# Kernel tuning notes

Hardware: AMD Instinct MI355X
Metric: run time of the kernel (lower is better)

## Reference

```python
import jax, jax.numpy as jnp
import numpy as np

N = 50000; E = 1600000; H = 128; R = 8; T = 2; P = 1000; M = 223


def setup_inputs() -> dict:
    key = jax.random.key(0)
    ks = jax.random.split(key, 16)
    s = 1.0 / np.sqrt(H).astype(np.float32)
    inp = {}
    inp['neigh_type_count'] = jax.random.uniform(ks[0], (N, 2), dtype=jnp.float32) * 5.0
    inp['norm'] = jax.random.uniform(ks[1], (E,), dtype=jnp.float32) + 0.1
    inp['special_cost'] = jax.random.uniform(ks[2], (N,), dtype=jnp.float32)
    inp['gt_map'] = jax.random.uniform(ks[3], (M, M), dtype=jnp.float32)
    inp['fc_w'] = jax.random.normal(ks[4], (2, H), dtype=jnp.float32) * (1.0 / np.sqrt(2.0))
    inp['fc_b'] = jnp.zeros((H,), jnp.float32)
    inp['w_nt'] = jax.random.normal(ks[5], (T, H, H), dtype=jnp.float32) * s
    inp['w_rel'] = jax.random.normal(ks[6], (R, H, H), dtype=jnp.float32) * s
    inp['fc2_w'] = jax.random.normal(ks[7], (H, 1), dtype=jnp.float32) * s
    inp['fc2_b'] = jnp.zeros((1,), jnp.float32)
    inp['fc3_w'] = jax.random.normal(ks[8], (H, 1), dtype=jnp.float32) * s
    inp['fc3_b'] = jnp.zeros((1,), jnp.float32)
    inp['fl3_w'] = jax.random.normal(ks[9], (H, P), dtype=jnp.float32) * s
    inp['fl3_b'] = jnp.zeros((P,), jnp.float32)
    inp['node_type'] = jax.random.randint(ks[10], (N,), 0, T, dtype=jnp.int32)
    inp['src'] = jax.random.randint(ks[11], (E,), 0, N, dtype=jnp.int32)
    inp['dst'] = jax.random.randint(ks[12], (E,), 0, N, dtype=jnp.int32)
    inp['etype'] = jax.random.randint(ks[13], (E,), 0, R, dtype=jnp.int32)
    return inp


def reference(neigh_type_count, norm, special_cost, gt_map, fc_w, fc_b, w_nt, w_rel,
              fc2_w, fc2_b, fc3_w, fc3_b, fl3_w, fl3_b, node_type, src, dst, etype):
    n = neigh_type_count.shape[0]
    # fc: [N,2] -> [N,H]
    h0 = neigh_type_count @ fc_w + fc_b
    # input RGCN layer: per-src-node-type transform, then per-edge-relation transform.
    # Compute node x type / node x relation products once, then gather per edge
    # (same math as per-edge bmm with gathered weights, far less traffic).
    h_nt_all = jnp.einsum('ni,tio->nto', h0, w_nt)                 # [N,T,H]
    h_nt = jnp.take_along_axis(h_nt_all, node_type[:, None, None].astype(jnp.int32), axis=1)[:, 0, :]  # [N,H]
    h_rel = jnp.einsum('ni,rio->nro', h_nt, w_rel)                 # [N,R,H]
    msg = h_rel[src, etype] * norm[:, None]                        # [E,H]
    h = jax.ops.segment_sum(msg, dst, num_segments=n)              # scatter-sum -> [N,H]
    h = jax.nn.relu(h)                                             # apply_func activation
    # fc2 + clamp(sigmoid)
    pred = jnp.clip(jax.nn.sigmoid(h @ fc2_w + fc2_b), 1e-7, 1e10) # [N,1]
    m = gt_map.shape[0]
    pm = pred[:m * m, 0].reshape(m, m)                             # pred node map [M,M]
    ce = -jnp.sum(gt_map * jnp.log2(pm))                           # min cross-entropy (single GT map)
    rs = jnp.sum(pm, axis=1)                                       # row sums [M]
    cs = jnp.sum(pm, axis=0)                                       # col sums [M]
    loss2 = jnp.sum(pm * (rs[:, None] - pm)) + jnp.sum(pm * (cs[None, :] - pm))
    sumone = jnp.sum((rs - 1.0) ** 2) + jnp.sum((cs - 1.0) ** 2)
    # fc_for_loss3 (sigmoid probs; summed so params get grads)
    prob3_sum = jnp.sum(jax.nn.sigmoid(h @ fl3_w + fl3_b))
    # OutputLayer: scatter-sum src pred_prob to dst, (sum-1)^2 * special_cost
    agg = jax.ops.segment_sum(pred[src, 0], dst, num_segments=n)
    out_cost = jnp.sum(((agg - 1.0) ** 2) * special_cost)
    # dgl.mean_nodes (single graph) + fc3
    gembed = jnp.mean(h, axis=0)
    pred_obj = (gembed @ fc3_w + fc3_b)[0]
    return jnp.stack([pred_obj, sumone, loss2, ce, out_cost, prob3_sum])
```

## Files before the change

### kernel.cpp

```cpp
#include <hip/hip_runtime.h>

#define H 128
#define RNUM 8
#define TNUM 2
#define PNUM 1000
#define MNUM 223
#define BNODES 64
#define NBUCK 782
#define BCAP 2304
#define EPB 8192

typedef __attribute__((ext_vector_type(8))) short bf16x8;
typedef __attribute__((ext_vector_type(4))) float f32x4;

__device__ __forceinline__ float fsig(float z) {
    return 1.0f / (1.0f + __expf(-z));
}
__device__ __forceinline__ float fsig_fast(float z) {
    return __builtin_amdgcn_rcpf(1.0f + __expf(-z));
}

__device__ __forceinline__ float wave_reduce(float v) {
#pragma unroll
    for (int off = 32; off > 0; off >>= 1) v += __shfl_down(v, off, 64);
    return v;
}

__device__ __forceinline__ unsigned short f2bf(float f) {
    unsigned int u = __float_as_uint(f);
    u += 0x7fffu + ((u >> 16) & 1u);
    return (unsigned short)(u >> 16);
}

__global__ void setup_kernel(const float* __restrict__ fl3_w, const float* __restrict__ fl3_b,
                             unsigned short* __restrict__ wt, float* __restrict__ biasws,
                             const float* __restrict__ fc_w, const float* __restrict__ fc_b,
                             const float* __restrict__ w_nt, const float* __restrict__ w_rel,
                             float* __restrict__ C) {
    __shared__ float G[3][H];
    int blk = blockIdx.x;
    int i = threadIdx.x;
    if (blk < 1024) {
        int p = blk;
        float v = (p < PNUM) ? fl3_w[(size_t)i * PNUM + p] : 0.0f;
        wt[(size_t)p * H + i] = f2bf(v);
        if (i == 0) biasws[p] = (p < PNUM) ? fl3_b[p] : -1.0e4f;
        return;
    }
    int tr = blk - 1024;
    int t = tr >> 3, r = tr & 7;
    float a0 = 0.f, a1 = 0.f, a2 = 0.f;
#pragma unroll 8
    for (int j = 0; j < H; ++j) {
        float w = w_nt[((size_t)t * H + j) * H + i];
        a0 += fc_w[j] * w;
        a1 += fc_w[H + j] * w;
        a2 += fc_b[j] * w;
    }
    G[0][i] = a0; G[1][i] = a1; G[2][i] = a2;
    __syncthreads();
    float c0 = 0.f, c1 = 0.f, c2 = 0.f;
#pragma unroll 8
    for (int k = 0; k < H; ++k) {
        float w = w_rel[((size_t)r * H + k) * H + i];
        c0 += G[0][k] * w;
        c1 += G[1][k] * w;
        c2 += G[2][k] * w;
    }
    C[((size_t)tr * 3 + 0) * H + i] = c0;
    C[((size_t)tr * 3 + 1) * H + i] = c1;
    C[((size_t)tr * 3 + 2) * H + i] = c2;
}

__global__ void cbt_kernel(const float* __restrict__ C, unsigned short* __restrict__ CbT) {
    int o = blockIdx.x;
    int k = threadIdx.x;
    CbT[o * 64 + k] = (k < 48) ? f2bf(C[k * 128 + o]) : (unsigned short)0;
}

__global__ __launch_bounds__(1024) void partition_kernel(
        const int* __restrict__ src, const int* __restrict__ dst,
        const int* __restrict__ etype, const float* __restrict__ norm,
        const int* __restrict__ node_type, int* __restrict__ cursor,
        uint2* __restrict__ buck, int E) {
    __shared__ int lh[NBUCK];
    __shared__ int gb[NBUCK];
    int tid = threadIdx.x;
    for (int i = tid; i < NBUCK; i += 1024) lh[i] = 0;
    __syncthreads();
    int base = blockIdx.x * EPB;
    uint2 pl[8]; int bb[8]; int rk[8];
#pragma unroll
    for (int c = 0; c < 8; ++c) {
        int e = base + c * 1024 + tid;
        bb[c] = -1;
        if (e < E) {
            int s = src[e];
            int d = dst[e];
            int r = etype[e];
            float nm = norm[e];
            int t = node_type[s];
            int b = d >> 6;
            int local = d & 63;
            pl[c].x = (unsigned)s | ((unsigned)local << 18) | ((unsigned)r << 24) | ((unsigned)t << 27);
            pl[c].y = __float_as_uint(nm);
            bb[c] = b;
            rk[c] = atomicAdd(&lh[b], 1);
        }
    }
    __syncthreads();
    for (int i = tid; i < NBUCK; i += 1024) {
        if (lh[i] > 0) {
            int g = atomicAdd(&cursor[i], lh[i]);
            gb[i] = (g < 0) ? 0 : (g > BCAP ? BCAP : g);
        }
    }
    __syncthreads();
#pragma unroll
    for (int c = 0; c < 8; ++c) {
        if (bb[c] >= 0) {
            int pos = gb[bb[c]] + rk[c];
            if (pos < BCAP) buck[(size_t)bb[c] * BCAP + pos] = pl[c];
        }
    }
}

__global__ __launch_bounds__(256) void bucket_node(
        const uint2* __restrict__ buck, const int* __restrict__ cursor,
        const float* __restrict__ ntc, const unsigned short* __restrict__ CbT,
        const float* __restrict__ fc2_w, const float* __restrict__ fc2_b,
        unsigned short* __restrict__ hb, float* __restrict__ pred,
        float* __restrict__ gpart, int N) {
    __shared__ float S[64 * 68];
    __shared__ unsigned short Cb[128 * 72];
    __shared__ float gloc[128];
    int tid = threadIdx.x;
    int bkt = blockIdx.x;
    for (int i = tid; i < 64 * 68; i += 256) S[i] = 0.0f;
    for (int g = tid; g < 1024; g += 256) {
        int row = g >> 3, c = g & 7;
        uint4 v = ((const uint4*)CbT)[g];
        *(uint4*)(Cb + row * 72 + c * 8) = v;
    }
    if (tid < 128) gloc[tid] = 0.0f;
    __syncthreads();

    int cnt = cursor[bkt];
    if (cnt > BCAP) cnt = BCAP;
    if (cnt < 0) cnt = 0;
    const uint2* bp = buck + (size_t)bkt * BCAP;
    for (int base = 0; base < cnt; base += 2048) {
        uint2 pl[8]; float2 cc[8]; int ii[8];
#pragma unroll
        for (int j = 0; j < 8; ++j) {
            ii[j] = base + j * 256 + tid;
            pl[j] = (ii[j] < cnt) ? bp[ii[j]] : make_uint2(0u, 0u);
        }
#pragma unroll
        for (int j = 0; j < 8; ++j)
            cc[j] = (ii[j] < cnt) ? ((const float2*)ntc)[pl[j].x & 0x3FFFF]
                                  : make_float2(0.f, 0.f);
#pragma unroll
        for (int j = 0; j < 8; ++j) {
            if (ii[j] < cnt) {
                int local = (pl[j].x >> 18) & 63;
                int tr = ((pl[j].x >> 24) & 7) + (((pl[j].x >> 27) & 1) << 3);
                float nm = __uint_as_float(pl[j].y);
                float* p = &S[local * 68 + tr * 3];
                atomicAdd(p, nm * cc[j].x);
                atomicAdd(p + 1, nm * cc[j].y);
                atomicAdd(p + 2, nm);
            }
        }
    }
    __syncthreads();

    int lane = tid & 63, w = tid >> 6;
    int lrow = lane & 15, quad = lane >> 4;

    bf16x8 a[2];
#pragma unroll
    for (int ks = 0; ks < 2; ++ks) {
        const float* sp = S + (w * 16 + lrow) * 68 + ks * 32 + quad * 8;
        float4 f0 = *(const float4*)sp;
        float4 f1 = *(const float4*)(sp + 4);
        bf16x8 t;
        t[0] = (short)f2bf(f0.x); t[1] = (short)f2bf(f0.y);
        t[2] = (short)f2bf(f0.z); t[3] = (short)f2bf(f0.w);
        t[4] = (short)f2bf(f1.x); t[5] = (short)f2bf(f1.y);
        t[6] = (short)f2bf(f1.z); t[7] = (short)f2bf(f1.w);
        a[ks] = t;
    }

    f32x4 acc[8];
#pragma unroll
    for (int tn = 0; tn < 8; ++tn) acc[tn] = (f32x4){0.f, 0.f, 0.f, 0.f};
#pragma unroll
    for (int ks = 0; ks < 2; ++ks) {
#pragma unroll
        for (int tn = 0; tn < 8; ++tn) {
            bf16x8 b = *(const bf16x8*)(Cb + (tn * 16 + lrow) * 72 + ks * 32 + quad * 8);
            acc[tn] = __builtin_amdgcn_mfma_f32_16x16x32_bf16(a[ks], b, acc[tn], 0, 0, 0);
        }
    }

#pragma unroll
    for (int tn = 0; tn < 8; ++tn)
#pragma unroll
        for (int r = 0; r < 4; ++r) acc[tn][r] = fmaxf(acc[tn][r], 0.f);

    int vbase = bkt * BNODES + w * 16 + quad * 4;
#pragma unroll
    for (int r = 0; r < 4; ++r) {
        unsigned short* hrow = hb + (size_t)(vbase + r) * H + lrow;
#pragma unroll
        for (int tn = 0; tn < 8; ++tn) hrow[tn * 16] = f2bf(acc[tn][r]);
    }
    float pd[4];
#pragma unroll
    for (int r = 0; r < 4; ++r) {
        float s = 0.f;
#pragma unroll
        for (int tn = 0; tn < 8; ++tn) s += acc[tn][r] * fc2_w[tn * 16 + lrow];
        pd[r] = s;
    }
#pragma unroll
    for (int mask = 1; mask < 16; mask <<= 1)
#pragma unroll
        for (int r = 0; r < 4; ++r) pd[r] += __shfl_xor(pd[r], mask, 64);
    if (lrow == 0) {
#pragma unroll
        for (int r = 0; r < 4; ++r) {
            int v = vbase + r;
            if (v < N) {
                float z = pd[r] + fc2_b[0];
                pred[v] = fminf(fmaxf(fsig(z), 1e-7f), 1e10f);
            }
        }
    }
    float csum[8];
#pragma unroll
    for (int tn = 0; tn < 8; ++tn)
        csum[tn] = acc[tn][0] + acc[tn][1] + acc[tn][2] + acc[tn][3];
#pragma unroll
    for (int mask = 16; mask < 64; mask <<= 1)
#pragma unroll
        for (int tn = 0; tn < 8; ++tn) csum[tn] += __shfl_xor(csum[tn], mask, 64);
    if (lane < 16) {
#pragma unroll
        for (int tn = 0; tn < 8; ++tn) atomicAdd(&gloc[tn * 16 + lrow], csum[tn]);
    }
    __syncthreads();
    if (tid < 128) gpart[(size_t)bkt * 128 + tid] = gloc[tid];
}

__global__ __launch_bounds__(256, 2) void mega_kernel(
        const unsigned short* __restrict__ hb, const unsigned short* __restrict__ wt,
        const float* __restrict__ biasws, float* __restrict__ psum, int nb128,
        const uint2* __restrict__ buck, const int* __restrict__ cursor,
        const float* __restrict__ pred, const float* __restrict__ sc,
        float* __restrict__ ocpart, int N,
        float* __restrict__ rs, float* __restrict__ cs,
        const float* __restrict__ gpart, float* __restrict__ gsum, int nbuck) {
    __shared__ unsigned short Bsh[128 * 136];
    __shared__ float red[8];
    int blk = blockIdx.x;
    int tid = threadIdx.x;
    int P1 = 2 * nb128;
    int P2 = P1 + nbuck;
    int P3 = P2 + 2 * MNUM;

    if (blk < P1) {
        int by = blk / nb128, bx = blk - by * nb128;
        int n0 = bx * 128;
        int pt0 = by * 4;
        int lane = tid & 63, wid = tid >> 6;
        int wy = wid >> 1, wx = wid & 1;
        int lrow = lane & 15, quad = lane >> 4;

        bf16x8 a[4][4];
#pragma unroll
        for (int tm = 0; tm < 4; ++tm) {
            const unsigned short* arow = hb + (size_t)(n0 + wy * 64 + tm * 16 + lrow) * H + quad * 8;
#pragma unroll
            for (int ks = 0; ks < 4; ++ks)
                a[tm][ks] = *(const bf16x8*)(arow + ks * 32);
        }

        float lsum = 0.f;
        for (int pi = 0; pi < 4; ++pi) {
            int pt = pt0 + pi;
            __syncthreads();
            {
                int c = tid & 15;
                int r0 = tid >> 4;
#pragma unroll
                for (int it = 0; it < 8; ++it) {
                    int row = r0 + it * 16;
                    uint4 bv = *(const uint4*)(wt + (size_t)(pt * 128 + row) * H + c * 8);
                    *(uint4*)(Bsh + row * 136 + c * 8) = bv;
                }
            }
            __syncthreads();

            f32x4 acc[4][4];
#pragma unroll
            for (int tm = 0; tm < 4; ++tm)
#pragma unroll
                for (int tn = 0; tn < 4; ++tn)
                    acc[tm][tn] = (f32x4){0.f, 0.f, 0.f, 0.f};

            const unsigned short* Bbase = Bsh + (wx * 64 + lrow) * 136 + quad * 8;
#pragma unroll
            for (int ks = 0; ks < 4; ++ks) {
                bf16x8 b[4];
#pragma unroll
                for (int tn = 0; tn < 4; ++tn)
                    b[tn] = *(const bf16x8*)(Bbase + tn * 16 * 136 + ks * 32);
#pragma unroll
                for (int tm = 0; tm < 4; ++tm)
#pragma unroll
                    for (int tn = 0; tn < 4; ++tn)
                        acc[tm][tn] = __builtin_amdgcn_mfma_f32_16x16x32_bf16(a[tm][ks], b[tn], acc[tm][tn], 0, 0, 0);
            }

#pragma unroll
            for (int tn = 0; tn < 4; ++tn) {
                float bv = biasws[pt * 128 + wx * 64 + tn * 16 + lrow];
#pragma unroll
                for (int tm = 0; tm < 4; ++tm) {
#pragma unroll
                    for (int r = 0; r < 4; ++r)
                        lsum += fsig_fast(acc[tm][tn][r] + bv);
                }
            }
        }
        lsum = wave_reduce(lsum);
        if (lane == 0) red[wid] = lsum;
        __syncthreads();
        if (tid == 0)
            psum[by * nb128 + bx] = red[0] + red[1] + red[2] + red[3];
    } else if (blk < P2) {
        int bkt = blk - P1;
        float* agg = (float*)Bsh;
        if (tid < BNODES) agg[tid] = 0.0f;
        __syncthreads();
        int cnt = cursor[bkt];
        if (cnt > BCAP) cnt = BCAP;
        if (cnt < 0) cnt = 0;
        const uint2* bp = buck + (size_t)bkt * BCAP;
        for (int base = 0; base < cnt; base += 2048) {
            unsigned x[8]; float pv[8]; int ii[8];
#pragma unroll
            for (int j = 0; j < 8; ++j) {
                ii[j] = base + j * 256 + tid;
                x[j] = (ii[j] < cnt) ? bp[ii[j]].x : 0u;
            }
#pragma unroll
            for (int j = 0; j < 8; ++j)
                pv[j] = (ii[j] < cnt) ? pred[x[j] & 0x3FFFF] : 0.f;
#pragma unroll
            for (int j = 0; j < 8; ++j)
                if (ii[j] < cnt) atomicAdd(&agg[(x[j] >> 18) & 63], pv[j]);
        }
        __syncthreads();
        if (tid < 64) {
            float v = 0.f;
            int node = bkt * BNODES + tid;
            if (node < N) {
                float d = agg[tid] - 1.0f;
                v = d * d * sc[node];
            }
            v = wave_reduce(v);
            if (tid == 0) ocpart[bkt] = v;
        }
    } else if (blk < P3) {
        int rc = blk - P2;
        float p = 0.f;
        if (rc < MNUM) {
            if (tid < MNUM) p = pred[rc * MNUM + tid];
        } else {
            int j = rc - MNUM;
            if (tid < MNUM) p = pred[tid * MNUM + j];
        }
        p = wave_reduce(p);
        if ((tid & 63) == 0) red[tid >> 6] = p;
        __syncthreads();
        if (tid == 0) {
            float s = red[0] + red[1] + red[2] + red[3];
            if (rc < MNUM) rs[rc] = s; else cs[rc - MNUM] = s;
        }
    } else {
        int dim = blk - P3;
        float s = 0.f;
        for (int b = tid; b < nbuck; b += 256) s += gpart[(size_t)b * 128 + dim];
        s = wave_reduce(s);
        if ((tid & 63) == 0) red[tid >> 6] = s;
        __syncthreads();
        if (tid == 0) gsum[dim] = red[0] + red[1] + red[2] + red[3];
    }
}

__global__ void losses_kernel(const float* __restrict__ pred, const float* __restrict__ gt,
                              const float* __restrict__ rs, const float* __restrict__ cs,
                              float* __restrict__ lce, float* __restrict__ ll2) {
    __shared__ float redc[4], redl[4];
    int blk = blockIdx.x, tid = threadIdx.x;
    float ce = 0.f, l2 = 0.f;
    if (tid < MNUM) {
        float p = pred[blk * MNUM + tid];
        ce = -gt[blk * MNUM + tid] * __log2f(p);
        l2 = p * (rs[blk] + cs[tid] - 2.0f * p);
    }
    ce = wave_reduce(ce);
    l2 = wave_reduce(l2);
    if ((tid & 63) == 0) { redc[tid >> 6] = ce; redl[tid >> 6] = l2; }
    __syncthreads();
    if (tid == 0) {
        lce[blk] = redc[0] + redc[1] + redc[2] + redc[3];
        ll2[blk] = redl[0] + redl[1] + redl[2] + redl[3];
    }
}

__global__ void tail_kernel(const float* __restrict__ rs, const float* __restrict__ cs,
                            const float* __restrict__ lce, const float* __restrict__ ll2,
                            const float* __restrict__ psum, int npsum,
                            const float* __restrict__ ocpart, int nbuck,
                            const float* __restrict__ gsum, const float* __restrict__ fc3_w,
                            const float* __restrict__ fc3_b, const float* __restrict__ fl3_b,
                            float* __restrict__ out, int N, int padrows) {
    __shared__ float red[4];
    int tid = threadIdx.x;
    float v = 0.f;
    if (tid < MNUM) {
        float a = rs[tid] - 1.0f, b = cs[tid] - 1.0f;
        v = a * a + b * b;
    }
    v = wave_reduce(v);
    if ((tid & 63) == 0) red[tid >> 6] = v;
    __syncthreads();
    if (tid == 0) out[1] = red[0] + red[1] + red[2] + red[3];
    __syncthreads();
    float ce = (tid < MNUM) ? lce[tid] : 0.f;
    ce = wave_reduce(ce);
    if ((tid & 63) == 0) red[tid >> 6] = ce;
    __syncthreads();
    if (tid == 0) out[3] = red[0] + red[1] + red[2] + red[3];
    __syncthreads();
    float l2 = (tid < MNUM) ? ll2[tid] : 0.f;
    l2 = wave_reduce(l2);
    if ((tid & 63) == 0) red[tid >> 6] = l2;
    __syncthreads();
    if (tid == 0) out[2] = red[0] + red[1] + red[2] + red[3];
    __syncthreads();
    float ps = 0.f;
    for (int i = tid; i < npsum; i += 256) ps += psum[i];
    float ss = 0.f;
    for (int p = tid; p < PNUM; p += 256) ss += fsig_fast(fl3_b[p]);
    float comb = ps - (float)padrows * ss;
    comb = wave_reduce(comb);
    if ((tid & 63) == 0) red[tid >> 6] = comb;
    __syncthreads();
    if (tid == 0) out[5] = red[0] + red[1] + red[2] + red[3];
    __syncthreads();
    float oc = 0.f;
    for (int b = tid; b < nbuck; b += 256) oc += ocpart[b];
    oc = wave_reduce(oc);
    if ((tid & 63) == 0) red[tid >> 6] = oc;
    __syncthreads();
    if (tid == 0) out[4] = red[0] + red[1] + red[2] + red[3];
    __syncthreads();
    float pv = 0.f;
    if (tid < 128) pv = gsum[tid] * (1.0f / (float)N) * fc3_w[tid];
    pv = wave_reduce(pv);
    if ((tid & 63) == 0) red[tid >> 6] = pv;
    __syncthreads();
    if (tid == 0) out[0] = red[0] + red[1] + fc3_b[0];
}

extern "C" void kernel_launch(void* const* d_in, const int* in_sizes, int n_in,
                              void* d_out, int out_size, void* d_ws, size_t ws_size,
                              hipStream_t stream) {
    const float* ntc   = (const float*)d_in[0];
    const float* norm  = (const float*)d_in[1];
    const float* sc    = (const float*)d_in[2];
    const float* gt    = (const float*)d_in[3];
    const float* fc_w  = (const float*)d_in[4];
    const float* fc_b  = (const float*)d_in[5];
    const float* w_nt  = (const float*)d_in[6];
    const float* w_rel = (const float*)d_in[7];
    const float* fc2_w = (const float*)d_in[8];
    const float* fc2_b = (const float*)d_in[9];
    const float* fc3_w = (const float*)d_in[10];
    const float* fc3_b = (const float*)d_in[11];
    const float* fl3_w = (const float*)d_in[12];
    const float* fl3_b = (const float*)d_in[13];
    const int* node_type = (const int*)d_in[14];
    const int* src   = (const int*)d_in[15];
    const int* dst   = (const int*)d_in[16];
    const int* etype = (const int*)d_in[17];
    int N = in_sizes[2];
    int E = in_sizes[1];
    int nb128 = (N + 127) / 128;
    int padN  = nb128 * 128;
    int nbuck = padN / BNODES;
    int npsum = nb128 * 2;

    float* ws   = (float*)d_ws;
    float* C    = ws;
    unsigned short* wt = (unsigned short*)(ws + 6144);
    float* biasws = ws + 71680;
    float* gsum = ws + 72704;
    float* rs   = ws + 72832;
    float* cs   = ws + 73088;
    int*  cursor = (int*)(ws + 73344);
    float* psum = ws + 74128;
    float* lce  = ws + 75152;
    float* ll2  = ws + 75408;
    float* ocpart = ws + 75664;
    unsigned short* CbT = (unsigned short*)(ws + 76688);
    float* gpart  = ws + 80784;
    float* pred = ws + 180880;
    unsigned short* hb = (unsigned short*)(pred + N);
    uint2* buck = (uint2*)(hb + (size_t)padN * H);
    float* out  = (float*)d_out;

    hipMemsetAsync(d_out, 0, 6 * sizeof(float), stream);
    hipMemsetAsync(cursor, 0, 784 * sizeof(int), stream);

    setup_kernel<<<1040, 128, 0, stream>>>(fl3_w, fl3_b, wt, biasws,
                                           fc_w, fc_b, w_nt, w_rel, C);
    cbt_kernel<<<128, 64, 0, stream>>>(C, CbT);
    partition_kernel<<<(E + EPB - 1) / EPB, 1024, 0, stream>>>(src, dst, etype, norm,
                                                               node_type, cursor, buck, E);
    bucket_node<<<nbuck, 256, 0, stream>>>(buck, cursor, ntc, CbT, fc2_w, fc2_b,
                                           hb, pred, gpart, N);
    int megablocks = 2 * nb128 + nbuck + 2 * MNUM + 128;
    mega_kernel<<<megablocks, 256, 0, stream>>>(hb, wt, biasws, psum, nb128,
                                                buck, cursor, pred, sc, ocpart, N,
                                                rs, cs, gpart, gsum, nbuck);
    losses_kernel<<<MNUM, 256, 0, stream>>>(pred, gt, rs, cs, lce, ll2);
    tail_kernel<<<1, 256, 0, stream>>>(rs, cs, lce, ll2, psum, npsum, ocpart, nbuck,
                                       gsum, fc3_w, fc3_b, fl3_b, out, N, padN - N);
}
```

Measured before the change: 238.6 us.

## Fold cbt and losses kernels into neighbors via algebraic loss2 rewrite

The setup kernel now writes the transposed bf16 CbT table directly, which removes the separate cbt_kernel launch. The loss2 term is rewritten as sum(rs^2)+sum(cs^2)-2*sum(p^2). That lets the row-sum blocks in mega_kernel also compute the cross-entropy and squared partials, so losses_kernel and its extra pass over pred are dropped. The bucket_node edge loop is also narrowed from 8 to 4 edges per thread per iteration. Two fewer launches cut launch and serialization overhead, but the algebraic form may differ slightly in float rounding.

```diff
diff --git a/kernel.cpp b/kernel.cpp
--- a/kernel.cpp
+++ b/kernel.cpp
@@ -36,7 +36,7 @@
                              unsigned short* __restrict__ wt, float* __restrict__ biasws,
                              const float* __restrict__ fc_w, const float* __restrict__ fc_b,
                              const float* __restrict__ w_nt, const float* __restrict__ w_rel,
-                             float* __restrict__ C) {
+                             unsigned short* __restrict__ CbT) {
     __shared__ float G[3][H];
     int blk = blockIdx.x;
     int i = threadIdx.x;
@@ -67,15 +67,14 @@
         c1 += G[1][k] * w;
         c2 += G[2][k] * w;
     }
-    C[((size_t)tr * 3 + 0) * H + i] = c0;
-    C[((size_t)tr * 3 + 1) * H + i] = c1;
-    C[((size_t)tr * 3 + 2) * H + i] = c2;
-}
-
-__global__ void cbt_kernel(const float* __restrict__ C, unsigned short* __restrict__ CbT) {
-    int o = blockIdx.x;
-    int k = threadIdx.x;
-    CbT[o * 64 + k] = (k < 48) ? f2bf(C[k * 128 + o]) : (unsigned short)0;
+    CbT[i * 64 + tr * 3 + 0] = f2bf(c0);
+    CbT[i * 64 + tr * 3 + 1] = f2bf(c1);
+    CbT[i * 64 + tr * 3 + 2] = f2bf(c2);
+    if (tr == 0) {
+        uint4 z = make_uint4(0u, 0u, 0u, 0u);
+        *(uint4*)(CbT + i * 64 + 48) = z;
+        *(uint4*)(CbT + i * 64 + 56) = z;
+    }
 }
 
 __global__ __launch_bounds__(1024) void partition_kernel(
@@ -149,19 +148,19 @@
     if (cnt > BCAP) cnt = BCAP;
     if (cnt < 0) cnt = 0;
     const uint2* bp = buck + (size_t)bkt * BCAP;
-    for (int base = 0; base < cnt; base += 2048) {
-        uint2 pl[8]; float2 cc[8]; int ii[8];
-#pragma unroll
-        for (int j = 0; j < 8; ++j) {
+    for (int base = 0; base < cnt; base += 1024) {
+        uint2 pl[4]; float2 cc[4]; int ii[4];
+#pragma unroll
+        for (int j = 0; j < 4; ++j) {
             ii[j] = base + j * 256 + tid;
             pl[j] = (ii[j] < cnt) ? bp[ii[j]] : make_uint2(0u, 0u);
         }
 #pragma unroll
-        for (int j = 0; j < 8; ++j)
+        for (int j = 0; j < 4; ++j)
             cc[j] = (ii[j] < cnt) ? ((const float2*)ntc)[pl[j].x & 0x3FFFF]
                                   : make_float2(0.f, 0.f);
 #pragma unroll
-        for (int j = 0; j < 8; ++j) {
+        for (int j = 0; j < 4; ++j) {
             if (ii[j] < cnt) {
                 int local = (pl[j].x >> 18) & 63;
                 int tr = ((pl[j].x >> 24) & 7) + (((pl[j].x >> 27) & 1) << 3);
@@ -259,11 +258,12 @@
         const float* __restrict__ biasws, float* __restrict__ psum, int nb128,
         const uint2* __restrict__ buck, const int* __restrict__ cursor,
         const float* __restrict__ pred, const float* __restrict__ sc,
-        float* __restrict__ ocpart, int N,
+        const float* __restrict__ gt, float* __restrict__ ocpart, int N,
         float* __restrict__ rs, float* __restrict__ cs,
+        float* __restrict__ cepart, float* __restrict__ sqpart,
         const float* __restrict__ gpart, float* __restrict__ gsum, int nbuck) {
     __shared__ unsigned short Bsh[128 * 136];
-    __shared__ float red[8];
+    __shared__ float red[12];
     int blk = blockIdx.x;
     int tid = threadIdx.x;
     int P1 = 2 * nb128;
@@ -376,19 +376,32 @@
         }
     } else if (blk < P3) {
         int rc = blk - P2;
-        float p = 0.f;
         if (rc < MNUM) {
-            if (tid < MNUM) p = pred[rc * MNUM + tid];
+            float p = 0.f, ce = 0.f, sq = 0.f;
+            if (tid < MNUM) {
+                p = pred[rc * MNUM + tid];
+                ce = -gt[rc * MNUM + tid] * __log2f(p);
+                sq = p * p;
+            }
+            p = wave_reduce(p);
+            ce = wave_reduce(ce);
+            sq = wave_reduce(sq);
+            int wid = tid >> 6;
+            if ((tid & 63) == 0) { red[wid] = p; red[4 + wid] = ce; red[8 + wid] = sq; }
+            __syncthreads();
+            if (tid == 0) {
+                rs[rc] = red[0] + red[1] + red[2] + red[3];
+                cepart[rc] = red[4] + red[5] + red[6] + red[7];
+                sqpart[rc] = red[8] + red[9] + red[10] + red[11];
+            }
         } else {
             int j = rc - MNUM;
+            float p = 0.f;
             if (tid < MNUM) p = pred[tid * MNUM + j];
-        }
-        p = wave_reduce(p);
-        if ((tid & 63) == 0) red[tid >> 6] = p;
-        __syncthreads();
-        if (tid == 0) {
-            float s = red[0] + red[1] + red[2] + red[3];
-            if (rc < MNUM) rs[rc] = s; else cs[rc - MNUM] = s;
+            p = wave_reduce(p);
+            if ((tid & 63) == 0) red[tid >> 6] = p;
+            __syncthreads();
+            if (tid == 0) cs[j] = red[0] + red[1] + red[2] + red[3];
         }
     } else {
         int dim = blk - P3;
@@ -401,29 +414,8 @@
     }
 }
 
-__global__ void losses_kernel(const float* __restrict__ pred, const float* __restrict__ gt,
-                              const float* __restrict__ rs, const float* __restrict__ cs,
-                              float* __restrict__ lce, float* __restrict__ ll2) {
-    __shared__ float redc[4], redl[4];
-    int blk = blockIdx.x, tid = threadIdx.x;
-    float ce = 0.f, l2 = 0.f;
-    if (tid < MNUM) {
-        float p = pred[blk * MNUM + tid];
-        ce = -gt[blk * MNUM + tid] * __log2f(p);
-        l2 = p * (rs[blk] + cs[tid] - 2.0f * p);
-    }
-    ce = wave_reduce(ce);
-    l2 = wave_reduce(l2);
-    if ((tid & 63) == 0) { redc[tid >> 6] = ce; redl[tid >> 6] = l2; }
-    __syncthreads();
-    if (tid == 0) {
-        lce[blk] = redc[0] + redc[1] + redc[2] + redc[3];
-        ll2[blk] = redl[0] + redl[1] + redl[2] + redl[3];
-    }
-}
-
 __global__ void tail_kernel(const float* __restrict__ rs, const float* __restrict__ cs,
-                            const float* __restrict__ lce, const float* __restrict__ ll2,
+                            const float* __restrict__ cepart, const float* __restrict__ sqpart,
                             const float* __restrict__ psum, int npsum,
                             const float* __restrict__ ocpart, int nbuck,
                             const float* __restrict__ gsum, const float* __restrict__ fc3_w,
@@ -441,13 +433,15 @@
     __syncthreads();
     if (tid == 0) out[1] = red[0] + red[1] + red[2] + red[3];
     __syncthreads();
-    float ce = (tid < MNUM) ? lce[tid] : 0.f;
+    float ce = (tid < MNUM) ? cepart[tid] : 0.f;
     ce = wave_reduce(ce);
     if ((tid & 63) == 0) red[tid >> 6] = ce;
     __syncthreads();
     if (tid == 0) out[3] = red[0] + red[1] + red[2] + red[3];
     __syncthreads();
-    float l2 = (tid < MNUM) ? ll2[tid] : 0.f;
+    float l2 = 0.f;
+    if (tid < MNUM)
+        l2 = rs[tid] * rs[tid] + cs[tid] * cs[tid] - 2.0f * sqpart[tid];
     l2 = wave_reduce(l2);
     if ((tid & 63) == 0) red[tid >> 6] = l2;
     __syncthreads();
@@ -507,20 +501,19 @@
     int npsum = nb128 * 2;
 
     float* ws   = (float*)d_ws;
-    float* C    = ws;
-    unsigned short* wt = (unsigned short*)(ws + 6144);
-    float* biasws = ws + 71680;
-    float* gsum = ws + 72704;
-    float* rs   = ws + 72832;
-    float* cs   = ws + 73088;
-    int*  cursor = (int*)(ws + 73344);
-    float* psum = ws + 74128;
-    float* lce  = ws + 75152;
-    float* ll2  = ws + 75408;
-    float* ocpart = ws + 75664;
-    unsigned short* CbT = (unsigned short*)(ws + 76688);
-    float* gpart  = ws + 80784;
-    float* pred = ws + 180880;
+    unsigned short* wt = (unsigned short*)ws;
+    float* biasws = ws + 65536;
+    float* gsum = ws + 66560;
+    float* rs   = ws + 66688;
+    float* cs   = ws + 66944;
+    int*  cursor = (int*)(ws + 67200);
+    float* psum = ws + 67984;
+    float* cepart = ws + 69008;
+    float* sqpart = ws + 69264;
+    float* ocpart = ws + 69520;
+    unsigned short* CbT = (unsigned short*)(ws + 70544);
+    float* gpart  = ws + 74640;
+    float* pred = ws + 174736;
     unsigned short* hb = (unsigned short*)(pred + N);
     uint2* buck = (uint2*)(hb + (size_t)padN * H);
     float* out  = (float*)d_out;
@@ -529,17 +522,15 @@
     hipMemsetAsync(cursor, 0, 784 * sizeof(int), stream);
 
     setup_kernel<<<1040, 128, 0, stream>>>(fl3_w, fl3_b, wt, biasws,
-                                           fc_w, fc_b, w_nt, w_rel, C);
-    cbt_kernel<<<128, 64, 0, stream>>>(C, CbT);
+                                           fc_w, fc_b, w_nt, w_rel, CbT);
     partition_kernel<<<(E + EPB - 1) / EPB, 1024, 0, stream>>>(src, dst, etype, norm,
                                                                node_type, cursor, buck, E);
     bucket_node<<<nbuck, 256, 0, stream>>>(buck, cursor, ntc, CbT, fc2_w, fc2_b,
                                            hb, pred, gpart, N);
     int megablocks = 2 * nb128 + nbuck + 2 * MNUM + 128;
     mega_kernel<<<megablocks, 256, 0, stream>>>(hb, wt, biasws, psum, nb128,
-                                                buck, cursor, pred, sc, ocpart, N,
-                                                rs, cs, gpart, gsum, nbuck);
-    losses_kernel<<<MNUM, 256, 0, stream>>>(pred, gt, rs, cs, lce, ll2);
-    tail_kernel<<<1, 256, 0, stream>>>(rs, cs, lce, ll2, psum, npsum, ocpart, nbuck,
+                                                buck, cursor, pred, sc, gt, ocpart, N,
+                                                rs, cs, cepart, sqpart, gpart, gsum, nbuck);
+    tail_kernel<<<1, 256, 0, stream>>>(rs, cs, cepart, sqpart, psum, npsum, ocpart, nbuck,
                                        gsum, fc3_w, fc3_b, fl3_b, out, N, padN - N);
 }
```

New measurement: 231.8 us. 1.03x faster.
